# Optimization experiments

Hardware: AMD Instinct MI355X
Metric: run time of the kernel (lower is better)

## Reference

```python
import jax, jax.numpy as jnp
import numpy as np

TEMP = 0.5
EPS = 1e-12  # matches torch F.normalize default eps


def _l2_normalize(x):
    n = jnp.sqrt(jnp.sum(x * x, axis=1, keepdims=True))
    return x / jnp.maximum(n, EPS)


def setup_inputs() -> dict:
    key = jax.random.key(0)
    k1, k2 = jax.random.split(key)
    B, D = 4096, 256
    return {
        "x_i": jax.random.normal(k1, (B, D), dtype=jnp.float32),
        "x_j": jax.random.normal(k2, (B, D), dtype=jnp.float32),
    }


def reference(x_i, x_j):
    B = x_i.shape[0]
    z = jnp.concatenate([_l2_normalize(x_i), _l2_normalize(x_j)], axis=0)  # [2B, D]
    # cosine similarity of normalized vectors == plain matmul
    sim = z @ z.T  # [2B, 2B]
    pos = jnp.concatenate([jnp.diagonal(sim, B), jnp.diagonal(sim, -B)], axis=0)  # [2B]
    neg_mask = 1.0 - jnp.eye(2 * B, dtype=sim.dtype)
    denom = jnp.sum(neg_mask * jnp.exp(sim / TEMP), axis=1)  # [2B]
    # -log(exp(pos/T) / denom) = -pos/T + log(denom)
    loss = jnp.sum(-(pos / TEMP) + jnp.log(denom)) / (2 * B)
    return loss
```

## Files before the change

### kernel.cpp

```cpp
#include <hip/hip_runtime.h>
#include <hip/hip_bf16.h>

#define B_ROWS 4096
#define NROWS  8192
#define D      256
#define TILES  64
#define NPAIRS 2080

typedef __attribute__((ext_vector_type(8))) short bf16x8;
typedef __attribute__((ext_vector_type(4))) float floatx4;

__device__ __forceinline__ void load16_to_lds(const short* g, short* l) {
    __builtin_amdgcn_global_load_lds(
        (const __attribute__((address_space(1))) unsigned int*)g,
        (__attribute__((address_space(3))) unsigned int*)l,
        16, 0, 0);
}

__global__ __launch_bounds__(256) void norm_pos_kernel(
    const float* __restrict__ xi, const float* __restrict__ xj,
    short* __restrict__ z, float* __restrict__ pos,
    float* __restrict__ selfdot) {
    int p    = blockIdx.x * 4 + (threadIdx.x >> 6);
    int lane = threadIdx.x & 63;
    float4 v1 = ((const float4*)(xi + (size_t)p * D))[lane];
    float4 v2 = ((const float4*)(xj + (size_t)p * D))[lane];
    float ss1 = v1.x * v1.x + v1.y * v1.y + v1.z * v1.z + v1.w * v1.w;
    float ss2 = v2.x * v2.x + v2.y * v2.y + v2.z * v2.z + v2.w * v2.w;
#pragma unroll
    for (int off = 32; off > 0; off >>= 1) {
        ss1 += __shfl_xor(ss1, off);
        ss2 += __shfl_xor(ss2, off);
    }
    float sc1 = 1.0f / fmaxf(sqrtf(ss1), 1e-12f);
    float sc2 = 1.0f / fmaxf(sqrtf(ss2), 1e-12f);

    union { __hip_bfloat16 h[4]; short4 s4; } u1, u2;
    u1.h[0] = __float2bfloat16(v1.x * sc1); u1.h[1] = __float2bfloat16(v1.y * sc1);
    u1.h[2] = __float2bfloat16(v1.z * sc1); u1.h[3] = __float2bfloat16(v1.w * sc1);
    u2.h[0] = __float2bfloat16(v2.x * sc2); u2.h[1] = __float2bfloat16(v2.y * sc2);
    u2.h[2] = __float2bfloat16(v2.z * sc2); u2.h[3] = __float2bfloat16(v2.w * sc2);
    ((short4*)(z + (size_t)p * D))[lane]            = u1.s4;
    ((short4*)(z + (size_t)(p + B_ROWS) * D))[lane] = u2.s4;

    float sd1 = 0.f, sd2 = 0.f, dp = 0.f;
#pragma unroll
    for (int j = 0; j < 4; j++) {
        float a = __bfloat162float(u1.h[j]);
        float b = __bfloat162float(u2.h[j]);
        sd1 += a * a; sd2 += b * b; dp += a * b;
    }
#pragma unroll
    for (int off = 32; off > 0; off >>= 1) {
        sd1 += __shfl_xor(sd1, off);
        sd2 += __shfl_xor(sd2, off);
        dp  += __shfl_xor(dp,  off);
    }
    if (lane == 0) {
        pos[p] = dp; pos[p + B_ROWS] = dp;
        selfdot[p] = sd1; selfdot[p + B_ROWS] = sd2;
    }
}

__global__ __launch_bounds__(256) void sim_rowsum_kernel(
    const short* __restrict__ z, float* __restrict__ rowsum) {
    __shared__ short As[4096];
    __shared__ short Bs[4096];
    __shared__ float rs_lds[128];
    __shared__ float cs_lds[128];

    int tid  = threadIdx.x;
    int lane = tid & 63;
    int w    = tid >> 6;
    int lm   = lane & 15;
    int lg   = lane >> 4;

    int bid = blockIdx.x;
    int ti  = (int)((129.0 - sqrt(16641.0 - 8.0 * (double)bid)) * 0.5);
    while (ti > 0 && ti * TILES - ti * (ti - 1) / 2 > bid) ti--;
    while ((ti + 1) * TILES - (ti + 1) * ti / 2 <= bid) ti++;
    int tj = ti + (bid - (ti * TILES - ti * (ti - 1) / 2));
    int m0 = ti * 128, n0 = tj * 128;

    int wr = (w & 1) * 64;
    int wc = (w >> 1) * 64;

    if (tid < 128) { rs_lds[tid] = 0.f; cs_lds[tid] = 0.f; }

    floatx4 acc[4][4];
#pragma unroll
    for (int mi = 0; mi < 4; mi++)
#pragma unroll
        for (int ni = 0; ni < 4; ni++) acc[mi][ni] = (floatx4){0.f, 0.f, 0.f, 0.f};

    for (int k0 = 0; k0 < D; k0 += 32) {
        __syncthreads();
#pragma unroll
        for (int c = 0; c < 2; c++) {
            int r = c * 64 + lane;
            load16_to_lds(z + (size_t)(m0 + r) * D + k0 + w * 8,
                          As + (w * 128 + c * 64) * 8);
            load16_to_lds(z + (size_t)(n0 + r) * D + k0 + w * 8,
                          Bs + (w * 128 + c * 64) * 8);
        }
        __syncthreads();

        bf16x8 a[4], b[4];
#pragma unroll
        for (int mi = 0; mi < 4; mi++)
            a[mi] = *(const bf16x8*)(As + (lg * 128 + wr + mi * 16 + lm) * 8);
#pragma unroll
        for (int ni = 0; ni < 4; ni++)
            b[ni] = *(const bf16x8*)(Bs + (lg * 128 + wc + ni * 16 + lm) * 8);
#pragma unroll
        for (int mi = 0; mi < 4; mi++)
#pragma unroll
            for (int ni = 0; ni < 4; ni++)
                acc[mi][ni] = __builtin_amdgcn_mfma_f32_16x16x32_bf16(
                    a[mi], b[ni], acc[mi][ni], 0, 0, 0);
    }

    float rs[4][4];
    float cs[4];
#pragma unroll
    for (int mi = 0; mi < 4; mi++)
#pragma unroll
        for (int r = 0; r < 4; r++) rs[mi][r] = 0.f;
#pragma unroll
    for (int ni = 0; ni < 4; ni++) cs[ni] = 0.f;

#pragma unroll
    for (int mi = 0; mi < 4; mi++)
#pragma unroll
        for (int ni = 0; ni < 4; ni++)
#pragma unroll
            for (int r = 0; r < 4; r++) {
                float e = __expf(2.0f * acc[mi][ni][r]);
                rs[mi][r] += e;
                cs[ni]    += e;
            }

    bool offdiag = (ti != tj);
#pragma unroll
    for (int mi = 0; mi < 4; mi++)
#pragma unroll
        for (int r = 0; r < 4; r++) {
            float s = rs[mi][r];
            s += __shfl_xor(s, 1); s += __shfl_xor(s, 2);
            s += __shfl_xor(s, 4); s += __shfl_xor(s, 8);
            if (lm == 0) atomicAdd(&rs_lds[wr + mi * 16 + lg * 4 + r], s);
        }
    if (offdiag) {
#pragma unroll
        for (int ni = 0; ni < 4; ni++) {
            float s = cs[ni];
            s += __shfl_xor(s, 16); s += __shfl_xor(s, 32);
            if (lane < 16) atomicAdd(&cs_lds[wc + ni * 16 + lm], s);
        }
    }
    __syncthreads();
    if (tid < 128) {
        atomicAdd(&rowsum[m0 + tid], rs_lds[tid]);
    } else if (offdiag) {
        atomicAdd(&rowsum[n0 + tid - 128], cs_lds[tid - 128]);
    }
}

__global__ void loss_kernel(const float* __restrict__ rowsum,
                            const float* __restrict__ pos,
                            const float* __restrict__ selfdot,
                            float* __restrict__ out) {
    int tid   = threadIdx.x;
    float acc = 0.f;
    for (int r = tid; r < NROWS; r += 256) {
        float denom = rowsum[r] - __expf(2.0f * selfdot[r]);
        acc += -2.0f * pos[r] + logf(denom);
    }
#pragma unroll
    for (int off = 32; off > 0; off >>= 1) acc += __shfl_xor(acc, off);
    __shared__ float sdata[4];
    int lane = tid & 63, w = tid >> 6;
    if (lane == 0) sdata[w] = acc;
    __syncthreads();
    if (tid == 0) {
        float t = sdata[0] + sdata[1] + sdata[2] + sdata[3];
        out[0]  = t / (float)NROWS;
    }
}

extern "C" void kernel_launch(void* const* d_in, const int* in_sizes, int n_in,
                              void* d_out, int out_size, void* d_ws, size_t ws_size,
                              hipStream_t stream) {
    const float* xi = (const float*)d_in[0];
    const float* xj = (const float*)d_in[1];
    float* out      = (float*)d_out;

    char* ws       = (char*)d_ws;
    short* z       = (short*)ws;
    float* rowsum  = (float*)(ws + (size_t)NROWS * D * 2);
    float* pos     = rowsum + NROWS;
    float* selfdot = pos + NROWS;

    hipMemsetAsync(rowsum, 0, NROWS * sizeof(float), stream);
    norm_pos_kernel<<<B_ROWS / 4, 256, 0, stream>>>(xi, xj, z, pos, selfdot);
    sim_rowsum_kernel<<<NPAIRS, 256, 0, stream>>>(z, rowsum);
    loss_kernel<<<1, 256, 0, stream>>>(rowsum, pos, selfdot, out);
}
```

Before: 121.8 us.

## Load MFMA operands directly from global, fuse memset and loss into other kernels

The GEMM tile kernel no longer stages operands through LDS. Each lane now loads its bf16x8 fragments straight from global memory with register double-buffering, which removes the per-k-step barriers. The memset is folded into the normalization kernel, and the final loss reduction runs in the last finishing block through an atomic counter, dropping two launches. The cost is uncoalesced 16-byte global loads repeated across waves instead of shared reuse, plus a serialized tail in one block.

```diff
diff --git a/kernel.cpp b/kernel.cpp
--- a/kernel.cpp
+++ b/kernel.cpp
@@ -10,17 +10,15 @@
 typedef __attribute__((ext_vector_type(8))) short bf16x8;
 typedef __attribute__((ext_vector_type(4))) float floatx4;
 
-__device__ __forceinline__ void load16_to_lds(const short* g, short* l) {
-    __builtin_amdgcn_global_load_lds(
-        (const __attribute__((address_space(1))) unsigned int*)g,
-        (__attribute__((address_space(3))) unsigned int*)l,
-        16, 0, 0);
-}
-
 __global__ __launch_bounds__(256) void norm_pos_kernel(
     const float* __restrict__ xi, const float* __restrict__ xj,
     short* __restrict__ z, float* __restrict__ pos,
-    float* __restrict__ selfdot) {
+    float* __restrict__ selfdot, float* __restrict__ rowsum,
+    float* __restrict__ out, unsigned int* __restrict__ counter) {
+    int gt = blockIdx.x * 256 + threadIdx.x;
+    if (gt < NROWS) rowsum[gt] = 0.f;
+    if (gt == 0) { out[0] = 0.f; counter[0] = 0u; }
+
     int p    = blockIdx.x * 4 + (threadIdx.x >> 6);
     int lane = threadIdx.x & 63;
     float4 v1 = ((const float4*)(xi + (size_t)p * D))[lane];
@@ -63,11 +61,13 @@
 }
 
 __global__ __launch_bounds__(256) void sim_rowsum_kernel(
-    const short* __restrict__ z, float* __restrict__ rowsum) {
-    __shared__ short As[4096];
-    __shared__ short Bs[4096];
+    const short* __restrict__ z, float* __restrict__ rowsum,
+    const float* __restrict__ pos, const float* __restrict__ selfdot,
+    unsigned int* __restrict__ counter, float* __restrict__ out) {
     __shared__ float rs_lds[128];
     __shared__ float cs_lds[128];
+    __shared__ unsigned int done_s;
+    __shared__ float sdata[4];
 
     int tid  = threadIdx.x;
     int lane = tid & 63;
@@ -87,37 +87,45 @@
 
     if (tid < 128) { rs_lds[tid] = 0.f; cs_lds[tid] = 0.f; }
 
+    const short* arow[4];
+    const short* brow[4];
+#pragma unroll
+    for (int mi = 0; mi < 4; mi++)
+        arow[mi] = z + (size_t)(m0 + wr + mi * 16 + lm) * D + lg * 8;
+#pragma unroll
+    for (int ni = 0; ni < 4; ni++)
+        brow[ni] = z + (size_t)(n0 + wc + ni * 16 + lm) * D + lg * 8;
+
     floatx4 acc[4][4];
 #pragma unroll
     for (int mi = 0; mi < 4; mi++)
 #pragma unroll
         for (int ni = 0; ni < 4; ni++) acc[mi][ni] = (floatx4){0.f, 0.f, 0.f, 0.f};
 
-    for (int k0 = 0; k0 < D; k0 += 32) {
-        __syncthreads();
-#pragma unroll
-        for (int c = 0; c < 2; c++) {
-            int r = c * 64 + lane;
-            load16_to_lds(z + (size_t)(m0 + r) * D + k0 + w * 8,
-                          As + (w * 128 + c * 64) * 8);
-            load16_to_lds(z + (size_t)(n0 + r) * D + k0 + w * 8,
-                          Bs + (w * 128 + c * 64) * 8);
-        }
-        __syncthreads();
-
-        bf16x8 a[4], b[4];
-#pragma unroll
-        for (int mi = 0; mi < 4; mi++)
-            a[mi] = *(const bf16x8*)(As + (lg * 128 + wr + mi * 16 + lm) * 8);
-#pragma unroll
-        for (int ni = 0; ni < 4; ni++)
-            b[ni] = *(const bf16x8*)(Bs + (lg * 128 + wc + ni * 16 + lm) * 8);
+    bf16x8 af[2][4], bf[2][4];
+#pragma unroll
+    for (int mi = 0; mi < 4; mi++) af[0][mi] = *(const bf16x8*)(arow[mi]);
+#pragma unroll
+    for (int ni = 0; ni < 4; ni++) bf[0][ni] = *(const bf16x8*)(brow[ni]);
+
+#pragma unroll
+    for (int it = 0; it < 8; it++) {
+        int cur = it & 1, nxt = cur ^ 1;
+        if (it < 7) {
+            int k = (it + 1) * 32;
+#pragma unroll
+            for (int mi = 0; mi < 4; mi++)
+                af[nxt][mi] = *(const bf16x8*)(arow[mi] + k);
+#pragma unroll
+            for (int ni = 0; ni < 4; ni++)
+                bf[nxt][ni] = *(const bf16x8*)(brow[ni] + k);
+        }
 #pragma unroll
         for (int mi = 0; mi < 4; mi++)
 #pragma unroll
             for (int ni = 0; ni < 4; ni++)
                 acc[mi][ni] = __builtin_amdgcn_mfma_f32_16x16x32_bf16(
-                    a[mi], b[ni], acc[mi][ni], 0, 0, 0);
+                    af[cur][mi], bf[cur][ni], acc[mi][ni], 0, 0, 0);
     }
 
     float rs[4][4];
@@ -164,27 +172,29 @@
     } else if (offdiag) {
         atomicAdd(&rowsum[n0 + tid - 128], cs_lds[tid - 128]);
     }
-}
-
-__global__ void loss_kernel(const float* __restrict__ rowsum,
-                            const float* __restrict__ pos,
-                            const float* __restrict__ selfdot,
-                            float* __restrict__ out) {
-    int tid   = threadIdx.x;
-    float acc = 0.f;
-    for (int r = tid; r < NROWS; r += 256) {
-        float denom = rowsum[r] - __expf(2.0f * selfdot[r]);
-        acc += -2.0f * pos[r] + logf(denom);
-    }
-#pragma unroll
-    for (int off = 32; off > 0; off >>= 1) acc += __shfl_xor(acc, off);
-    __shared__ float sdata[4];
-    int lane = tid & 63, w = tid >> 6;
-    if (lane == 0) sdata[w] = acc;
+
     __syncthreads();
     if (tid == 0) {
-        float t = sdata[0] + sdata[1] + sdata[2] + sdata[3];
-        out[0]  = t / (float)NROWS;
+        __threadfence();
+        done_s = atomicAdd(counter, 1u);
+    }
+    __syncthreads();
+    if (done_s == (unsigned int)(NPAIRS - 1)) {
+        __threadfence();
+        float acc_l = 0.f;
+#pragma unroll 4
+        for (int r = tid; r < NROWS; r += 256) {
+            float rsv = __hip_atomic_load(&rowsum[r], __ATOMIC_RELAXED,
+                                          __HIP_MEMORY_SCOPE_AGENT);
+            float denom = rsv - __expf(2.0f * selfdot[r]);
+            acc_l += -2.0f * pos[r] + logf(denom);
+        }
+#pragma unroll
+        for (int off = 32; off > 0; off >>= 1) acc_l += __shfl_xor(acc_l, off);
+        if (lane == 0) sdata[w] = acc_l;
+        __syncthreads();
+        if (tid == 0)
+            out[0] = (sdata[0] + sdata[1] + sdata[2] + sdata[3]) / (float)NROWS;
     }
 }
 
@@ -195,14 +205,15 @@
     const float* xj = (const float*)d_in[1];
     float* out      = (float*)d_out;
 
-    char* ws       = (char*)d_ws;
-    short* z       = (short*)ws;
-    float* rowsum  = (float*)(ws + (size_t)NROWS * D * 2);
-    float* pos     = rowsum + NROWS;
-    float* selfdot = pos + NROWS;
-
-    hipMemsetAsync(rowsum, 0, NROWS * sizeof(float), stream);
-    norm_pos_kernel<<<B_ROWS / 4, 256, 0, stream>>>(xi, xj, z, pos, selfdot);
-    sim_rowsum_kernel<<<NPAIRS, 256, 0, stream>>>(z, rowsum);
-    loss_kernel<<<1, 256, 0, stream>>>(rowsum, pos, selfdot, out);
+    char* ws        = (char*)d_ws;
+    short* z        = (short*)ws;
+    float* rowsum   = (float*)(ws + (size_t)NROWS * D * 2);
+    float* pos      = rowsum + NROWS;
+    float* selfdot  = pos + NROWS;
+    unsigned int* counter = (unsigned int*)(selfdot + NROWS);
+
+    norm_pos_kernel<<<B_ROWS / 4, 256, 0, stream>>>(xi, xj, z, pos, selfdot,
+                                                    rowsum, out, counter);
+    sim_rowsum_kernel<<<NPAIRS, 256, 0, stream>>>(z, rowsum, pos, selfdot,
+                                                  counter, out);
 }
```

Result: slower. 156.6 us (+28.6%).
